# Performance work log

Hardware: AMD Instinct MI355X
Metric: run time of the kernel (lower is better)

The kernel has to match this reference:

```python
import jax, jax.numpy as jnp
import numpy as np

C = 299792458.0
FC = 9.7e9
BW = 300e6 * 16
TCOH = 10.0 * 16
LAMBDA1 = C / FC                 # ~0.0309 m
RANGE_RES = C / BW / 2.0 * 5.0   # ~0.156 m
GRID = 100


def _gaussian_pdf(x, mu, sigma):
    return jnp.exp(-0.5 * ((x - mu) / sigma) ** 2)


def setup_inputs() -> dict:
    key = jax.random.key(0)
    k1, k2, k3, k4 = jax.random.split(key, 4)
    B, N = 4, 8000
    return {
        "sampled_points": jax.random.normal(k1, (B, N, 3), dtype=jnp.float32),
        "point_normals": jax.random.normal(k2, (B, N, 3), dtype=jnp.float32),
        "RadarLos": jax.random.normal(k3, (1, 3), dtype=jnp.float32),
        "SpinAxis": jax.random.normal(k4, (1, 3), dtype=jnp.float32),
        "Omega": jnp.ones((1, 1), dtype=jnp.float32),
    }


def reference(sampled_points, point_normals, RadarLos, SpinAxis, Omega):
    # range-doppler grid, shape [100, 100] (torch indexing='xy')
    range_map, dopple_map = jnp.meshgrid(
        jnp.linspace(-10.0, 10.0, GRID, dtype=jnp.float32),
        jnp.linspace(-3.0, 3.0, GRID, dtype=jnp.float32),
        indexing="xy",
    )

    # point kinematics
    point_vel = jnp.cross(SpinAxis[:, None, :], sampled_points)          # [B,N,3]
    point_vel_radial = Omega * jnp.sum(RadarLos[:, None, :] * point_vel, axis=2)  # [B,N]
    point_doppler = -2.0 * point_vel_radial / LAMBDA1                    # [B,N]
    point_range = jnp.sum(RadarLos[:, None, :] * sampled_points, axis=2)  # [B,N]
    point_amp = jnp.clip(
        -4.0 * jnp.sum(RadarLos[:, None, :] * point_normals, axis=2), 0.0, 1.0
    )  # [B,N]

    doppler_res = LAMBDA1 / 2.0 / Omega / TCOH  # [1,1], broadcasts over grid

    # per-point 2D gaussian splat: [B,N,100,100] then reduce over N
    g_range = _gaussian_pdf(point_range[:, :, None, None], range_map[None, None], RANGE_RES)
    g_dop = _gaussian_pdf(point_doppler[:, :, None, None], dopple_map[None, None], doppler_res)
    image = jnp.sum(point_amp[:, :, None, None] * g_range * g_dop, axis=1)  # [B,100,100]
    return image
```

## Files before the change

### kernel.cpp

```cpp
#include <hip/hip_runtime.h>
#include <math.h>

#define NGRID 100

__global__ __launch_bounds__(256) void isar_splat(
        const float* __restrict__ pts,
        const float* __restrict__ nrm,
        const float* __restrict__ los,
        const float* __restrict__ spin,
        const float* __restrict__ omega,
        float* __restrict__ out,
        int BN, int N) {
    int idx = blockIdx.x * blockDim.x + threadIdx.x;
    if (idx >= BN) return;

    const double L0 = (double)los[0], L1 = (double)los[1], L2 = (double)los[2];
    const double S0 = (double)spin[0], S1 = (double)spin[1], S2 = (double)spin[2];
    const double Om = (double)omega[0];

    const float* pp = pts + (size_t)idx * 3;
    const float* nn = nrm + (size_t)idx * 3;
    const double p0 = (double)pp[0], p1 = (double)pp[1], p2 = (double)pp[2];
    const double n0 = (double)nn[0], n1 = (double)nn[1], n2 = (double)nn[2];

    double amp = -4.0 * (L0 * n0 + L1 * n1 + L2 * n2);
    if (!(amp > 0.0)) return;
    amp = fmin(amp, 1.0);

    double v0 = S1 * p2 - S2 * p1;
    double v1 = S2 * p0 - S0 * p2;
    double v2 = S0 * p1 - S1 * p0;
    double vrad = Om * (L0 * v0 + L1 * v1 + L2 * v2);

    const double LAM = 299792458.0 / 9.7e9;
    double dop = -2.0 * vrad / LAM;
    double rng = L0 * p0 + L1 * p1 + L2 * p2;

    double dsig = LAM / 2.0 / Om / 160.0;
    const double rsig = 299792458.0 / 4.8e9 / 2.0 * 5.0;

    const double CUT = 10.0;

    double ddlo = (dop - CUT * dsig + 3.0) * (99.0 / 6.0);
    double ddhi = (dop + CUT * dsig + 3.0) * (99.0 / 6.0);
    if (ddhi < -1.0 || ddlo > (double)(NGRID + 1)) return;
    int i0 = max(0, (int)floor(ddlo) - 1);
    int i1 = min(NGRID - 1, (int)ceil(ddhi) + 1);
    if (i0 > i1) return;

    double rrlo = (rng - CUT * rsig + 10.0) * (99.0 / 20.0);
    double rrhi = (rng + CUT * rsig + 10.0) * (99.0 / 20.0);
    if (rrhi < -1.0 || rrlo > (double)(NGRID + 1)) return;
    int j0 = max(0, (int)floor(rrlo) - 1);
    int j1 = min(NGRID - 1, (int)ceil(rrhi) + 1);
    if (j0 > j1) return;

    int b = idx / N;
    float* outb = out + (size_t)b * NGRID * NGRID;

    for (int i = i0; i <= i1; ++i) {
        double dbin = -3.0 + (double)i * (6.0 / 99.0);
        double qd = (dop - dbin) / dsig;
        double gd = exp(-0.5 * qd * qd);
        if (gd == 0.0) continue;
        for (int j = j0; j <= j1; ++j) {
            double rbin = -10.0 + (double)j * (20.0 / 99.0);
            double qr = (rng - rbin) / rsig;
            double gr = exp(-0.5 * qr * qr);
            double c = amp * gr * gd;
            float cf = (float)c;
            if (cf != 0.0f)
                atomicAdd(&outb[i * NGRID + j], cf);
        }
    }
}

extern "C" void kernel_launch(void* const* d_in, const int* in_sizes, int n_in,
                              void* d_out, int out_size, void* d_ws, size_t ws_size,
                              hipStream_t stream) {
    const float* pts  = (const float*)d_in[0];
    const float* nrm  = (const float*)d_in[1];
    const float* los  = (const float*)d_in[2];
    const float* spin = (const float*)d_in[3];
    const float* om   = (const float*)d_in[4];
    float* out = (float*)d_out;

    int BN = in_sizes[0] / 3;
    int B  = out_size / (NGRID * NGRID);
    if (B < 1) B = 1;
    int N  = BN / B;

    hipMemsetAsync(d_out, 0, (size_t)out_size * sizeof(float), stream);

    int threads = 256;
    int blocks = (BN + threads - 1) / threads;
    isar_splat<<<blocks, threads, 0, stream>>>(pts, nrm, los, spin, om, out, BN, N);
}
```

Before: 15.95 us.

## Convert scatter splat to per-row gather with shared-memory accumulation

Replaces the per-point scatter kernel, which used global atomics, with one block per (batch, doppler row). Each block scans all points of its batch, drops those outside the row's doppler window, and accumulates range contributions into a shared-memory row. The row is then written out directly, so the memset and global atomic contention go away. In exchange every block rereads and recomputes kinematics for all N points, so 400 blocks each process 8000 points in double precision.

```diff
diff --git a/kernel.cpp b/kernel.cpp
--- a/kernel.cpp
+++ b/kernel.cpp
@@ -3,76 +3,77 @@
 
 #define NGRID 100
 
-__global__ __launch_bounds__(256) void isar_splat(
+__global__ __launch_bounds__(256) void isar_gather(
         const float* __restrict__ pts,
         const float* __restrict__ nrm,
         const float* __restrict__ los,
         const float* __restrict__ spin,
         const float* __restrict__ omega,
         float* __restrict__ out,
-        int BN, int N) {
-    int idx = blockIdx.x * blockDim.x + threadIdx.x;
-    if (idx >= BN) return;
+        int N) {
+    const int blk = blockIdx.x;
+    const int b = blk / NGRID;
+    const int i = blk % NGRID;
+
+    __shared__ float row[NGRID];
+    for (int t = threadIdx.x; t < NGRID; t += blockDim.x) row[t] = 0.0f;
+    __syncthreads();
 
     const double L0 = (double)los[0], L1 = (double)los[1], L2 = (double)los[2];
     const double S0 = (double)spin[0], S1 = (double)spin[1], S2 = (double)spin[2];
     const double Om = (double)omega[0];
 
-    const float* pp = pts + (size_t)idx * 3;
-    const float* nn = nrm + (size_t)idx * 3;
-    const double p0 = (double)pp[0], p1 = (double)pp[1], p2 = (double)pp[2];
-    const double n0 = (double)nn[0], n1 = (double)nn[1], n2 = (double)nn[2];
-
-    double amp = -4.0 * (L0 * n0 + L1 * n1 + L2 * n2);
-    if (!(amp > 0.0)) return;
-    amp = fmin(amp, 1.0);
-
-    double v0 = S1 * p2 - S2 * p1;
-    double v1 = S2 * p0 - S0 * p2;
-    double v2 = S0 * p1 - S1 * p0;
-    double vrad = Om * (L0 * v0 + L1 * v1 + L2 * v2);
-
     const double LAM = 299792458.0 / 9.7e9;
-    double dop = -2.0 * vrad / LAM;
-    double rng = L0 * p0 + L1 * p1 + L2 * p2;
-
-    double dsig = LAM / 2.0 / Om / 160.0;
+    const double dsig = LAM / 2.0 / Om / 160.0;
     const double rsig = 299792458.0 / 4.8e9 / 2.0 * 5.0;
-
+    const double dbin = -3.0 + (double)i * (6.0 / 99.0);
     const double CUT = 10.0;
 
-    double ddlo = (dop - CUT * dsig + 3.0) * (99.0 / 6.0);
-    double ddhi = (dop + CUT * dsig + 3.0) * (99.0 / 6.0);
-    if (ddhi < -1.0 || ddlo > (double)(NGRID + 1)) return;
-    int i0 = max(0, (int)floor(ddlo) - 1);
-    int i1 = min(NGRID - 1, (int)ceil(ddhi) + 1);
-    if (i0 > i1) return;
+    const float* ppb = pts + (size_t)b * N * 3;
+    const float* nnb = nrm + (size_t)b * N * 3;
 
-    double rrlo = (rng - CUT * rsig + 10.0) * (99.0 / 20.0);
-    double rrhi = (rng + CUT * rsig + 10.0) * (99.0 / 20.0);
-    if (rrhi < -1.0 || rrlo > (double)(NGRID + 1)) return;
-    int j0 = max(0, (int)floor(rrlo) - 1);
-    int j1 = min(NGRID - 1, (int)ceil(rrhi) + 1);
-    if (j0 > j1) return;
+    for (int n = threadIdx.x; n < N; n += blockDim.x) {
+        const float* pp = ppb + (size_t)n * 3;
+        const double p0 = (double)pp[0], p1 = (double)pp[1], p2 = (double)pp[2];
 
-    int b = idx / N;
-    float* outb = out + (size_t)b * NGRID * NGRID;
+        const double v0 = S1 * p2 - S2 * p1;
+        const double v1 = S2 * p0 - S0 * p2;
+        const double v2 = S0 * p1 - S1 * p0;
+        const double vrad = Om * (L0 * v0 + L1 * v1 + L2 * v2);
+        const double dop = -2.0 * vrad / LAM;
 
-    for (int i = i0; i <= i1; ++i) {
-        double dbin = -3.0 + (double)i * (6.0 / 99.0);
-        double qd = (dop - dbin) / dsig;
-        double gd = exp(-0.5 * qd * qd);
-        if (gd == 0.0) continue;
+        const double qd = (dop - dbin) / dsig;
+        if (fabs(qd) > 14.5) continue;
+
+        const double rng = L0 * p0 + L1 * p1 + L2 * p2;
+
+        const double rrlo = (rng - CUT * rsig + 10.0) * (99.0 / 20.0);
+        const double rrhi = (rng + CUT * rsig + 10.0) * (99.0 / 20.0);
+        if (rrhi < -1.0 || rrlo > (double)(NGRID + 1)) continue;
+        const int j0 = max(0, (int)floor(rrlo) - 1);
+        const int j1 = min(NGRID - 1, (int)ceil(rrhi) + 1);
+        if (j0 > j1) continue;
+
+        const float* nn = nnb + (size_t)n * 3;
+        double amp = -4.0 * (L0 * (double)nn[0] + L1 * (double)nn[1] +
+                             L2 * (double)nn[2]);
+        if (!(amp > 0.0)) continue;
+        amp = fmin(amp, 1.0);
+
+        const double gd = exp(-0.5 * qd * qd);
+
         for (int j = j0; j <= j1; ++j) {
-            double rbin = -10.0 + (double)j * (20.0 / 99.0);
-            double qr = (rng - rbin) / rsig;
-            double gr = exp(-0.5 * qr * qr);
-            double c = amp * gr * gd;
-            float cf = (float)c;
-            if (cf != 0.0f)
-                atomicAdd(&outb[i * NGRID + j], cf);
+            const double rbin = -10.0 + (double)j * (20.0 / 99.0);
+            const double qr = (rng - rbin) / rsig;
+            const double gr = exp(-0.5 * qr * qr);
+            const float cf = (float)(amp * gr * gd);
+            if (cf != 0.0f) atomicAdd(&row[j], cf);
         }
     }
+
+    __syncthreads();
+    float* outb = out + ((size_t)b * NGRID + i) * NGRID;
+    for (int t = threadIdx.x; t < NGRID; t += blockDim.x) outb[t] = row[t];
 }
 
 extern "C" void kernel_launch(void* const* d_in, const int* in_sizes, int n_in,
@@ -90,9 +91,5 @@
     if (B < 1) B = 1;
     int N  = BN / B;
 
-    hipMemsetAsync(d_out, 0, (size_t)out_size * sizeof(float), stream);
-
-    int threads = 256;
-    int blocks = (BN + threads - 1) / threads;
-    isar_splat<<<blocks, threads, 0, stream>>>(pts, nrm, los, spin, om, out, BN, N);
+    isar_gather<<<B * NGRID, 256, 0, stream>>>(pts, nrm, los, spin, om, out, N);
 }
```

After: 17.03 us. 6.8% more time.
